# Kernel optimization log

Measured on AMD Instinct MI355X. Metric: run time of the kernel, lower is better.

## Reference

```python
import jax, jax.numpy as jnp
import numpy as np

WINDOW = 20  # window_size from init

def setup_inputs() -> dict:
    key = jax.random.key(0)
    ks = jax.random.split(key, 8)
    B, K, L, H = 8, 64, 1024, 256
    FFN = 3 * H * 4  # input_dim*ffn_ratio
    cand_span_reps = jax.random.normal(ks[0], (B, K, H), dtype=jnp.float32)
    token_reps = jax.random.normal(ks[1], (B, L, H), dtype=jnp.float32)
    W1 = jax.random.normal(ks[2], (3 * H, FFN), dtype=jnp.float32) * (1.0 / np.sqrt(3 * H))
    b1 = jnp.zeros((FFN,), dtype=jnp.float32)
    W2 = jax.random.normal(ks[3], (FFN, H), dtype=jnp.float32) * (1.0 / np.sqrt(FFN))
    b2 = jnp.zeros((H,), dtype=jnp.float32)
    cand_span_ids = jnp.sort(jax.random.randint(ks[4], (B, K, 2), 0, L), axis=-1)
    token_masks = jnp.ones((B, L), dtype=bool)
    return {"cand_span_reps": cand_span_reps, "token_reps": token_reps,
            "W1": W1, "b1": b1, "W2": W2, "b2": b2,
            "cand_span_ids": cand_span_ids, "token_masks": token_masks}

def _span_window_max(token_reps, span_ids, token_masks, window):
    # token_reps: [B,L,H]; span_ids: [B,K,2]; token_masks: [B,L]
    L = token_reps.shape[1]
    seq = jnp.arange(L)[None, None, :]                      # [1,1,L]
    start = span_ids[:, :, 0][:, :, None]                   # [B,K,1]
    end = span_ids[:, :, 1][:, :, None]                     # [B,K,1]
    mask = (((seq >= start - window) & (seq < start)) |
            ((seq > end) & (seq <= end + window)))
    mask = mask & token_masks[:, None, :]                   # [B,K,L]
    # masked max over L -> [B,K,H]
    filled = jnp.where(mask[..., None], token_reps[:, None, :, :], -jnp.inf)
    return jnp.max(filled, axis=2)

def reference(cand_span_reps, token_reps, W1, b1, W2, b2, cand_span_ids, token_masks):
    B, K, H = cand_span_reps.shape
    # Per-span pooled window context [B,K,H]. The pairwise context over the
    # UNION of head & tail windows equals the elementwise max of the two
    # per-span window maxes (max over A|B == max(max A, max B)).
    ctx = _span_window_max(token_reps, cand_span_ids, token_masks, WINDOW)
    context_reps = jnp.maximum(ctx[:, :, None, :], ctx[:, None, :, :])   # [B,K,K,H]
    head_reps = jnp.broadcast_to(cand_span_reps[:, :, None, :], (B, K, K, H))
    tail_reps = jnp.broadcast_to(cand_span_reps[:, None, :, :], (B, K, K, H))
    rel = jnp.concatenate([head_reps, tail_reps, context_reps], axis=-1)  # [B,K,K,3H]
    h = jax.nn.relu(jnp.einsum('bijd,df->bijf', rel, W1) + b1)
    out = jnp.einsum('bijf,fh->bijh', h, W2) + b2
    return out.reshape(B, K * K, H)
```

## Files before the change

kernel.cpp:

```cpp
#include <hip/hip_runtime.h>
#include <hip/hip_bf16.h>
#include <cstdint>
#include <cstddef>


typedef __attribute__((ext_vector_type(8))) short short8;
typedef __attribute__((ext_vector_type(4))) float f32x4;
typedef __attribute__((ext_vector_type(2))) unsigned int u32x2;

#define B_DIM 8
#define K_DIM 64
#define H_DIM 256
#define L_DIM 1024
#define FFN_DIM 3072
#define WINDOW 20

__device__ __forceinline__ unsigned short f2b(float f) {
  unsigned int u = __float_as_uint(f);
  unsigned int r = (u + 0x7FFFu + ((u >> 16) & 1u)) >> 16;
  return (unsigned short)r;
}
__device__ __forceinline__ float b2f(unsigned short h) {
  return __uint_as_float(((unsigned int)h) << 16);
}
__device__ __forceinline__ f32x4 zero4() {
  f32x4 z = {0.f, 0.f, 0.f, 0.f};
  return z;
}
__device__ __forceinline__ void gload_lds16(const void* g, void* l) {
  __builtin_amdgcn_global_load_lds(
      (const __attribute__((address_space(1))) void*)g,
      (__attribute__((address_space(3))) void*)l, 16, 0, 0);
}
__device__ __forceinline__ unsigned int cvt_pk_bf16(float lo, float hi) {
  unsigned int r;
  asm("v_cvt_pk_bf16_f32 %0, %1, %2" : "=v"(r) : "v"(lo), "v"(hi));
  return r;
}


__global__ void cvt_bf16_kernel(const float* __restrict__ in,
                                unsigned short* __restrict__ out, int n) {
  int i = blockIdx.x * blockDim.x + threadIdx.x;
  if (i < n) out[i] = f2b(in[i]);
}

__global__ void transpose_cvt_kernel(const float* __restrict__ in,
                                     unsigned short* __restrict__ out,
                                     int R, int C) {
  __shared__ float t[64][65];
  int c0 = blockIdx.x * 64, r0 = blockIdx.y * 64;
  int tr = threadIdx.x >> 6, tc = threadIdx.x & 63;
  for (int rr = tr; rr < 64; rr += 4)
    t[rr][tc] = in[(size_t)(r0 + rr) * C + (c0 + tc)];
  __syncthreads();
  for (int cc = tr; cc < 64; cc += 4)
    out[(size_t)(c0 + cc) * R + (r0 + tc)] = f2b(t[tc][cc]);
}

__global__ void ctx_kernel(const float* __restrict__ token,
                           const int* __restrict__ ids,
                           unsigned short* __restrict__ ctx) {
  int bk = blockIdx.x;
  int b = bk >> 6;
  int h = threadIdx.x;
  int s = ids[bk * 2 + 0];
  int e = ids[bk * 2 + 1];
  const float* tb = token + ((size_t)b * L_DIM) * H_DIM + h;
  float m = -INFINITY;
  int lo = s - WINDOW; if (lo < 0) lo = 0;
  for (int l2 = lo; l2 < s; ++l2) m = fmaxf(m, tb[(size_t)l2 * H_DIM]);
  int hi = e + WINDOW; if (hi > L_DIM - 1) hi = L_DIM - 1;
  for (int l2 = e + 1; l2 <= hi; ++l2) m = fmaxf(m, tb[(size_t)l2 * H_DIM]);
  ctx[(size_t)bk * H_DIM + h] = f2b(m);
}

__global__ __launch_bounds__(256) void at_gemm_kernel(
    const unsigned short* __restrict__ candb,
    const unsigned short* __restrict__ w1abt,
    const float* __restrict__ b1, float* __restrict__ AT) {
  int n0 = blockIdx.x * 64;
  int r0 = blockIdx.y * 64;
  __shared__ __align__(16) unsigned short A[64 * 256];
  int w = threadIdx.x >> 6, l = threadIdx.x & 63;
  int l15 = l & 15, l4 = l >> 4;
  {
    int row = w * 16 + l15;
    const short8* src = (const short8*)(candb + (size_t)(r0 + row) * H_DIM);
    #pragma unroll
    for (int t = 0; t < 8; ++t) {
      int u = l4 + 4 * t;
      short8 v = src[u];
      *(short8*)(A + row * 256 + ((u ^ (row & 7)) * 8)) = v;
    }
  }
  __syncthreads();
  f32x4 acc[4] = {zero4(), zero4(), zero4(), zero4()};
  int n = n0 + 16 * w + l15;
  const unsigned short* bp = w1abt + (size_t)n * H_DIM + l4 * 8;
  #pragma unroll
  for (int kk = 0; kk < 8; ++kk) {
    short8 bfrag = *(const short8*)(bp + kk * 32);
    #pragma unroll
    for (int rf = 0; rf < 4; ++rf) {
      int row = rf * 16 + l15;
      int u = kk * 4 + l4;
      short8 afrag = *(const short8*)(A + row * 256 + ((u ^ (row & 7)) * 8));
      acc[rf] = __builtin_amdgcn_mfma_f32_16x16x32_bf16(afrag, bfrag, acc[rf], 0, 0, 0);
    }
  }
  float bias = (n < FFN_DIM) ? b1[n] : 0.0f;
  #pragma unroll
  for (int rf = 0; rf < 4; ++rf) {
    #pragma unroll
    for (int qq = 0; qq < 4; ++qq) {
      int row = r0 + rf * 16 + l4 * 4 + qq;
      AT[(size_t)row * (2 * FFN_DIM) + n] = acc[rf][qq] + bias;
    }
  }
}

__global__ __launch_bounds__(512, 4) void fused_kernel(
    const unsigned short* __restrict__ ctx,
    const unsigned short* __restrict__ w1ct,
    const unsigned short* __restrict__ w2t,
    const float* __restrict__ AT,
    const float* __restrict__ b2,
    float* __restrict__ out) {
  int blk = blockIdx.x;
  blk = (blk & 7) * 64 + (blk >> 3);
  int b = blk >> 6, i = blk & 63;

  __shared__ __align__(16) char W1s[2 * 16384];
  __shared__ __align__(16) char W2s[2 * 16384];
  __shared__ __align__(16) char HcS[2 * 4096];

  int tid = threadIdx.x;
  int w = tid >> 6, l = tid & 63;
  int l15 = l & 15, l4 = l >> 4;
  int wl = l15 & 7;
  int s3 = (l15 >> 1) & 3;

  if (w < 4) {
    int wf = w & 1, wj2 = w >> 1;
    int jloc = 32 * wj2 + l15;

    short8 bfr[8][2];
    {
      const unsigned short* cb = ctx + ((size_t)b * K_DIM) * H_DIM;
      const unsigned short* ci = cb + (size_t)i * H_DIM;
      #pragma unroll
      for (int kk = 0; kk < 8; ++kk) {
        int hoff = kk * 32 + l4 * 8;
        short8 vi = *(const short8*)(ci + hoff);
        #pragma unroll
        for (int jb = 0; jb < 2; ++jb) {
          short8 vj = *(const short8*)(cb + (size_t)(jloc + jb * 16) * H_DIM + hoff);
          short8 vm;
          #pragma unroll
          for (int e = 0; e < 8; ++e) {
            float fa = b2f((unsigned short)vi[e]);
            float fb = b2f((unsigned short)vj[e]);
            vm[e] = (fa >= fb) ? vi[e] : vj[e];
          }
          bfr[kk][jb] = vm;
        }
      }
    }

    int baseA = (16 * wf + l15) * 512;
    int offAe = (l4 ^ wl) << 4;
    int offAo = ((4 + l4) ^ wl) << 4;
    int uW = 2 * wf + (l4 >> 1);
    int offHw = jloc * 64 + ((uW ^ s3) << 4) + ((l4 & 1) << 3);

    const float* avp  = AT + (size_t)(b * K_DIM + i) * (2 * FFN_DIM) + 16 * wf + 4 * l4;
    const float* tvp0 = AT + (size_t)(b * K_DIM + jloc) * (2 * FFN_DIM) + FFN_DIM + 16 * wf + 4 * l4;
    const float* tvp1 = tvp0 + (size_t)16 * (2 * FFN_DIM);

    __builtin_amdgcn_s_barrier();
    __builtin_amdgcn_sched_barrier(0);

    for (int c = 0; c <= 96; ++c) {
      if (c < 96) {
        f32x4 av  = *(const f32x4*)avp;
        f32x4 tv0 = *(const f32x4*)tvp0;
        f32x4 tv1 = *(const f32x4*)tvp1;
        avp += 32; tvp0 += 32; tvp1 += 32;
        __builtin_amdgcn_sched_barrier(0);

        const char* w1p = &W1s[(c & 1) * 16384 + baseA];
        f32x4 acc1[2] = {zero4(), zero4()};
        __builtin_amdgcn_s_setprio(1);
        #pragma unroll
        for (int m = 0; m < 4; ++m) {
          short8 afe = *(const short8*)(w1p + m * 128 + offAe);
          acc1[0] = __builtin_amdgcn_mfma_f32_16x16x32_bf16(afe, bfr[2 * m][0], acc1[0], 0, 0, 0);
          acc1[1] = __builtin_amdgcn_mfma_f32_16x16x32_bf16(afe, bfr[2 * m][1], acc1[1], 0, 0, 0);
          short8 afo = *(const short8*)(w1p + m * 128 + offAo);
          acc1[0] = __builtin_amdgcn_mfma_f32_16x16x32_bf16(afo, bfr[2 * m + 1][0], acc1[0], 0, 0, 0);
          acc1[1] = __builtin_amdgcn_mfma_f32_16x16x32_bf16(afo, bfr[2 * m + 1][1], acc1[1], 0, 0, 0);
        }
        __builtin_amdgcn_s_setprio(0);

        char* hw = &HcS[(c & 1) * 4096];
        {
          float v0 = fmaxf(acc1[0][0] + av[0] + tv0[0], 0.0f);
          float v1 = fmaxf(acc1[0][1] + av[1] + tv0[1], 0.0f);
          float v2 = fmaxf(acc1[0][2] + av[2] + tv0[2], 0.0f);
          float v3 = fmaxf(acc1[0][3] + av[3] + tv0[3], 0.0f);
          u32x2 pk;
          pk.x = cvt_pk_bf16(v0, v1);
          pk.y = cvt_pk_bf16(v2, v3);
          *(u32x2*)(hw + offHw) = pk;
        }
        {
          float v0 = fmaxf(acc1[1][0] + av[0] + tv1[0], 0.0f);
          float v1 = fmaxf(acc1[1][1] + av[1] + tv1[1], 0.0f);
          float v2 = fmaxf(acc1[1][2] + av[2] + tv1[2], 0.0f);
          float v3 = fmaxf(acc1[1][3] + av[3] + tv1[3], 0.0f);
          u32x2 pk;
          pk.x = cvt_pk_bf16(v0, v1);
          pk.y = cvt_pk_bf16(v2, v3);
          *(u32x2*)(hw + offHw + 1024) = pk;
        }
      }

      __builtin_amdgcn_sched_barrier(0);
      asm volatile("s_waitcnt vmcnt(0) lgkmcnt(0)" ::: "memory");
      __builtin_amdgcn_sched_barrier(0);
      __builtin_amdgcn_s_barrier();
      __builtin_amdgcn_sched_barrier(0);
    }
  } else {
    int ch = w - 4;
    int tid_c = (ch << 6) | l;

    int fr = tid_c >> 5, u32i = tid_c & 31;
    int offW1 = fr * 512 + (((u32i & 24) | ((u32i & 7) ^ (fr & 7))) << 4);
    int h2 = tid_c >> 2, u2 = tid_c & 3;
    int offW2 = h2 * 6144 + ((u2 ^ ((h2 >> 1) & 3)) << 4);

    const char* gW1 = (const char*)w1ct + offW1;
    const char* gW2 = (const char*)w2t + offW2;
    char* dW1base = &W1s[tid_c * 16];
    char* dW2base = &W2s[tid_c * 16];

    int baseW2 = ch * 4096 + l15 * 64 + ((l4 ^ s3) << 4);
    int baseHr = l15 * 64 + ((l4 ^ s3) << 4);

    f32x4 accO[4][4];
    #pragma unroll
    for (int cf = 0; cf < 4; ++cf)
      #pragma unroll
      for (int jt = 0; jt < 4; ++jt) accO[cf][jt] = zero4();

    {
      gload_lds16(gW1, dW1base);
      gload_lds16(gW1 + 4096, dW1base + 4096);
      gload_lds16(gW1 + 8192, dW1base + 8192);
      gload_lds16(gW1 + 12288, dW1base + 12288);
      gW1 += 16384;
    }
    __builtin_amdgcn_sched_barrier(0);
    asm volatile("s_waitcnt vmcnt(0)" ::: "memory");
    __builtin_amdgcn_sched_barrier(0);
    __builtin_amdgcn_s_barrier();
    __builtin_amdgcn_sched_barrier(0);

    for (int c = 0; c <= 96; ++c) {
      if (c < 95) {
        char* d = dW1base + ((c + 1) & 1) * 16384;
        gload_lds16(gW1, d);
        gload_lds16(gW1 + 4096, d + 4096);
        gload_lds16(gW1 + 8192, d + 8192);
        gload_lds16(gW1 + 12288, d + 12288);
        gW1 += 16384;
      }
      if (c < 96) {
        char* d = dW2base + (c & 1) * 16384;
        gload_lds16(gW2, d);
        gload_lds16(gW2 + 1 * 393216, d + 4096);
        gload_lds16(gW2 + 2 * 393216, d + 8192);
        gload_lds16(gW2 + 3 * 393216, d + 12288);
        gW2 += 64;
      }
      __builtin_amdgcn_sched_barrier(0);

      if (c > 0) {
        const char* w2p = &W2s[((c - 1) & 1) * 16384];
        const char* hcp = &HcS[((c - 1) & 1) * 4096];
        short8 wfr[4], hbv[4];
        #pragma unroll
        for (int cf = 0; cf < 4; ++cf)
          wfr[cf] = *(const short8*)(w2p + baseW2 + cf * 1024);
        #pragma unroll
        for (int jt = 0; jt < 4; ++jt)
          hbv[jt] = *(const short8*)(hcp + baseHr + jt * 1024);
        __builtin_amdgcn_s_setprio(1);
        #pragma unroll
        for (int cf = 0; cf < 4; ++cf)
          #pragma unroll
          for (int jt = 0; jt < 4; ++jt)
            accO[cf][jt] = __builtin_amdgcn_mfma_f32_16x16x32_bf16(wfr[cf], hbv[jt], accO[cf][jt], 0, 0, 0);
        __builtin_amdgcn_s_setprio(0);
      }

      __builtin_amdgcn_sched_barrier(0);
      asm volatile("s_waitcnt vmcnt(0) lgkmcnt(0)" ::: "memory");
      __builtin_amdgcn_sched_barrier(0);
      __builtin_amdgcn_s_barrier();
      __builtin_amdgcn_sched_barrier(0);
    }

    f32x4 bv[4];
    #pragma unroll
    for (int cf = 0; cf < 4; ++cf)
      bv[cf] = *(const f32x4*)(b2 + 64 * ch + cf * 16 + 4 * l4);
    #pragma unroll
    for (int jt = 0; jt < 4; ++jt) {
      int j = jt * 16 + l15;
      float* row = out + ((size_t)b * (K_DIM * K_DIM) + (size_t)i * K_DIM + j) * H_DIM;
      #pragma unroll
      for (int cf = 0; cf < 4; ++cf) {
        f32x4 v = accO[cf][jt] + bv[cf];
        *(f32x4*)(row + 64 * ch + cf * 16 + 4 * l4) = v;
      }
    }
  }
}


extern "C" void kernel_launch(void* const* d_in, const int* in_sizes, int n_in,
                              void* d_out, int out_size, void* d_ws, size_t ws_size,
                              hipStream_t stream) {
  const float* cand  = (const float*)d_in[0];
  const float* token = (const float*)d_in[1];
  const float* W1    = (const float*)d_in[2];
  const float* b1    = (const float*)d_in[3];
  const float* W2    = (const float*)d_in[4];
  const float* b2    = (const float*)d_in[5];
  const int*   ids   = (const int*)d_in[6];
  float* out = (float*)d_out;

  char* ws = (char*)d_ws;
  unsigned short* ctx   = (unsigned short*)(ws);
  unsigned short* candb = (unsigned short*)(ws + 262144);
  unsigned short* w1abt = (unsigned short*)(ws + 524288);
  unsigned short* w1ct  = (unsigned short*)(ws + 3670016);
  unsigned short* w2t   = (unsigned short*)(ws + 5242880);
  float*          AT    = (float*)(ws + 6815744);

  hipLaunchKernelGGL(cvt_bf16_kernel, dim3(512), dim3(256), 0, stream,
                     cand, candb, B_DIM * K_DIM * H_DIM);
  hipLaunchKernelGGL(transpose_cvt_kernel, dim3(48, 4), dim3(256), 0, stream,
                     W1, w1abt, 256, FFN_DIM);
  hipLaunchKernelGGL(transpose_cvt_kernel, dim3(48, 4), dim3(256), 0, stream,
                     W1 + (size_t)256 * FFN_DIM, w1abt + (size_t)FFN_DIM * 256, 256, FFN_DIM);
  hipLaunchKernelGGL(transpose_cvt_kernel, dim3(48, 4), dim3(256), 0, stream,
                     W1 + (size_t)512 * FFN_DIM, w1ct, 256, FFN_DIM);
  hipLaunchKernelGGL(transpose_cvt_kernel, dim3(4, 48), dim3(256), 0, stream,
                     W2, w2t, FFN_DIM, 256);
  hipLaunchKernelGGL(ctx_kernel, dim3(512), dim3(256), 0, stream, token, ids, ctx);
  hipLaunchKernelGGL(at_gemm_kernel, dim3(96, 8), dim3(256), 0, stream,
                     candb, w1abt, b1, AT);
  hipLaunchKernelGGL(fused_kernel, dim3(512), dim3(512), 0, stream,
                     ctx, w1ct, w2t, AT, b2, out);
}
```

Before: 181.2 us.

## Load W2 fragments directly into registers instead of staging through LDS

The consumer waves now read W2 MFMA fragments straight from global memory into double-buffered registers (even/odd), and the 32 KB W2 LDS buffer is removed. The loop is unrolled by two so each buffer is refilled one step ahead, and the wait becomes vmcnt(4) so the in-flight W2 loads can overlap the barrier. This removes an LDS write/read round trip and frees shared memory, which could raise occupancy. In exchange it issues uncoalesced 16-byte strided global loads (rows are FFN_DIM apart) that depend on L2 hits, and it assumes the vmcnt ordering is correct.

```diff
diff --git a/kernel.cpp b/kernel.cpp
--- a/kernel.cpp
+++ b/kernel.cpp
@@ -132,7 +132,6 @@
   int b = blk >> 6, i = blk & 63;
 
   __shared__ __align__(16) char W1s[2 * 16384];
-  __shared__ __align__(16) char W2s[2 * 16384];
   __shared__ __align__(16) char HcS[2 * 4096];
 
   int tid = threadIdx.x;
@@ -238,15 +237,11 @@
 
     int fr = tid_c >> 5, u32i = tid_c & 31;
     int offW1 = fr * 512 + (((u32i & 24) | ((u32i & 7) ^ (fr & 7))) << 4);
-    int h2 = tid_c >> 2, u2 = tid_c & 3;
-    int offW2 = h2 * 6144 + ((u2 ^ ((h2 >> 1) & 3)) << 4);
-
     const char* gW1 = (const char*)w1ct + offW1;
-    const char* gW2 = (const char*)w2t + offW2;
     char* dW1base = &W1s[tid_c * 16];
-    char* dW2base = &W2s[tid_c * 16];
-
-    int baseW2 = ch * 4096 + l15 * 64 + ((l4 ^ s3) << 4);
+
+    const unsigned short* w2r = w2t + (size_t)(64 * ch + l15) * FFN_DIM + l4 * 8;
+
     int baseHr = l15 * 64 + ((l4 ^ s3) << 4);
 
     f32x4 accO[4][4];
@@ -255,62 +250,73 @@
       #pragma unroll
       for (int jt = 0; jt < 4; ++jt) accO[cf][jt] = zero4();
 
-    {
-      gload_lds16(gW1, dW1base);
-      gload_lds16(gW1 + 4096, dW1base + 4096);
-      gload_lds16(gW1 + 8192, dW1base + 8192);
-      gload_lds16(gW1 + 12288, dW1base + 12288);
+    short8 wfE[4], wfO[4];
+
+    auto stageW1 = [&](char* d) {
+      gload_lds16(gW1, d);
+      gload_lds16(gW1 + 4096, d + 4096);
+      gload_lds16(gW1 + 8192, d + 8192);
+      gload_lds16(gW1 + 12288, d + 12288);
       gW1 += 16384;
-    }
-    __builtin_amdgcn_sched_barrier(0);
-    asm volatile("s_waitcnt vmcnt(0)" ::: "memory");
-    __builtin_amdgcn_sched_barrier(0);
-    __builtin_amdgcn_s_barrier();
-    __builtin_amdgcn_sched_barrier(0);
-
-    for (int c = 0; c <= 96; ++c) {
-      if (c < 95) {
-        char* d = dW1base + ((c + 1) & 1) * 16384;
-        gload_lds16(gW1, d);
-        gload_lds16(gW1 + 4096, d + 4096);
-        gload_lds16(gW1 + 8192, d + 8192);
-        gload_lds16(gW1 + 12288, d + 12288);
-        gW1 += 16384;
-      }
-      if (c < 96) {
-        char* d = dW2base + (c & 1) * 16384;
-        gload_lds16(gW2, d);
-        gload_lds16(gW2 + 1 * 393216, d + 4096);
-        gload_lds16(gW2 + 2 * 393216, d + 8192);
-        gload_lds16(gW2 + 3 * 393216, d + 12288);
-        gW2 += 64;
-      }
-      __builtin_amdgcn_sched_barrier(0);
-
-      if (c > 0) {
-        const char* w2p = &W2s[((c - 1) & 1) * 16384];
-        const char* hcp = &HcS[((c - 1) & 1) * 4096];
-        short8 wfr[4], hbv[4];
-        #pragma unroll
-        for (int cf = 0; cf < 4; ++cf)
-          wfr[cf] = *(const short8*)(w2p + baseW2 + cf * 1024);
+    };
+    auto loadW2 = [&](short8 (&buf)[4]) {
+      buf[0] = *(const short8*)(w2r);
+      buf[1] = *(const short8*)(w2r + (size_t)16 * FFN_DIM);
+      buf[2] = *(const short8*)(w2r + (size_t)32 * FFN_DIM);
+      buf[3] = *(const short8*)(w2r + (size_t)48 * FFN_DIM);
+      w2r += 32;
+    };
+    auto runG2 = [&](int cprev, short8 (&wfr)[4]) {
+      const char* hcp = &HcS[(cprev & 1) * 4096];
+      short8 hbv[4];
+      #pragma unroll
+      for (int jt = 0; jt < 4; ++jt)
+        hbv[jt] = *(const short8*)(hcp + baseHr + jt * 1024);
+      __builtin_amdgcn_s_setprio(1);
+      #pragma unroll
+      for (int cf = 0; cf < 4; ++cf)
         #pragma unroll
         for (int jt = 0; jt < 4; ++jt)
-          hbv[jt] = *(const short8*)(hcp + baseHr + jt * 1024);
-        __builtin_amdgcn_s_setprio(1);
-        #pragma unroll
-        for (int cf = 0; cf < 4; ++cf)
-          #pragma unroll
-          for (int jt = 0; jt < 4; ++jt)
-            accO[cf][jt] = __builtin_amdgcn_mfma_f32_16x16x32_bf16(wfr[cf], hbv[jt], accO[cf][jt], 0, 0, 0);
-        __builtin_amdgcn_s_setprio(0);
-      }
-
-      __builtin_amdgcn_sched_barrier(0);
-      asm volatile("s_waitcnt vmcnt(0) lgkmcnt(0)" ::: "memory");
+          accO[cf][jt] = __builtin_amdgcn_mfma_f32_16x16x32_bf16(wfr[cf], hbv[jt], accO[cf][jt], 0, 0, 0);
+      __builtin_amdgcn_s_setprio(0);
+    };
+    auto endbar = [&]() {
+      __builtin_amdgcn_sched_barrier(0);
+      asm volatile("s_waitcnt vmcnt(4) lgkmcnt(0)" ::: "memory");
       __builtin_amdgcn_sched_barrier(0);
       __builtin_amdgcn_s_barrier();
       __builtin_amdgcn_sched_barrier(0);
+    };
+
+    stageW1(dW1base);
+    loadW2(wfE);
+    __builtin_amdgcn_sched_barrier(0);
+    asm volatile("s_waitcnt vmcnt(0)" ::: "memory");
+    __builtin_amdgcn_sched_barrier(0);
+    __builtin_amdgcn_s_barrier();
+    __builtin_amdgcn_sched_barrier(0);
+
+    stageW1(dW1base + 16384);
+    __builtin_amdgcn_sched_barrier(0);
+    loadW2(wfO);
+    endbar();
+
+    for (int p = 0; p < 48; ++p) {
+      int c1 = 2 * p + 1;
+      if (c1 + 1 <= 95) stageW1(dW1base + (((c1 + 1) & 1) * 16384));
+      __builtin_amdgcn_sched_barrier(0);
+      runG2(c1 - 1, wfE);
+      __builtin_amdgcn_sched_barrier(0);
+      if (c1 + 1 <= 95) loadW2(wfE);
+      endbar();
+
+      int c2 = 2 * p + 2;
+      if (c2 + 1 <= 95) stageW1(dW1base + (((c2 + 1) & 1) * 16384));
+      __builtin_amdgcn_sched_barrier(0);
+      runG2(c2 - 1, wfO);
+      __builtin_amdgcn_sched_barrier(0);
+      if (c2 + 1 <= 95) loadW2(wfO);
+      endbar();
     }
 
     f32x4 bv[4];
```

Result: slower. 224.5 us (+23.9%).

## Halve GEMM1 producer waves and store head/tail FFN partials as bf16

Applied to the files above, without the earlier changes.

The fused kernel drops from four to two first-stage producer waves. Each producer now covers all 64 j-rows, issuing four MFMA accumulators per W1 fragment and holding twice the context fragments in registers. The block shrinks to 384 threads with launch bounds allowing three blocks per CU. The precomputed head/tail partial activations (AT) are written and read as bf16 instead of fp32, which halves that global traffic but adds rounding error before the ReLU.

```diff
diff --git a/kernel.cpp b/kernel.cpp
--- a/kernel.cpp
+++ b/kernel.cpp
@@ -7,6 +7,7 @@
 typedef __attribute__((ext_vector_type(8))) short short8;
 typedef __attribute__((ext_vector_type(4))) float f32x4;
 typedef __attribute__((ext_vector_type(2))) unsigned int u32x2;
+typedef __attribute__((ext_vector_type(4))) unsigned short u16x4;
 
 #define B_DIM 8
 #define K_DIM 64
@@ -78,7 +79,7 @@
 __global__ __launch_bounds__(256) void at_gemm_kernel(
     const unsigned short* __restrict__ candb,
     const unsigned short* __restrict__ w1abt,
-    const float* __restrict__ b1, float* __restrict__ AT) {
+    const float* __restrict__ b1, unsigned short* __restrict__ ATb) {
   int n0 = blockIdx.x * 64;
   int r0 = blockIdx.y * 64;
   __shared__ __align__(16) unsigned short A[64 * 256];
@@ -115,16 +116,16 @@
     #pragma unroll
     for (int qq = 0; qq < 4; ++qq) {
       int row = r0 + rf * 16 + l4 * 4 + qq;
-      AT[(size_t)row * (2 * FFN_DIM) + n] = acc[rf][qq] + bias;
+      ATb[(size_t)row * (2 * FFN_DIM) + n] = f2b(acc[rf][qq] + bias);
     }
   }
 }
 
-__global__ __launch_bounds__(512, 4) void fused_kernel(
+__global__ __launch_bounds__(384, 3) void fused_kernel(
     const unsigned short* __restrict__ ctx,
     const unsigned short* __restrict__ w1ct,
     const unsigned short* __restrict__ w2t,
-    const float* __restrict__ AT,
+    const unsigned short* __restrict__ ATb,
     const float* __restrict__ b2,
     float* __restrict__ out) {
   int blk = blockIdx.x;
@@ -141,11 +142,10 @@
   int wl = l15 & 7;
   int s3 = (l15 >> 1) & 3;
 
-  if (w < 4) {
-    int wf = w & 1, wj2 = w >> 1;
-    int jloc = 32 * wj2 + l15;
-
-    short8 bfr[8][2];
+  if (w < 2) {
+    int wf = w;
+
+    short8 bfr[8][4];
     {
       const unsigned short* cb = ctx + ((size_t)b * K_DIM) * H_DIM;
       const unsigned short* ci = cb + (size_t)i * H_DIM;
@@ -154,8 +154,8 @@
         int hoff = kk * 32 + l4 * 8;
         short8 vi = *(const short8*)(ci + hoff);
         #pragma unroll
-        for (int jb = 0; jb < 2; ++jb) {
-          short8 vj = *(const short8*)(cb + (size_t)(jloc + jb * 16) * H_DIM + hoff);
+        for (int jb = 0; jb < 4; ++jb) {
+          short8 vj = *(const short8*)(cb + (size_t)(jb * 16 + l15) * H_DIM + hoff);
           short8 vm;
           #pragma unroll
           for (int e = 0; e < 8; ++e) {
@@ -172,58 +172,75 @@
     int offAe = (l4 ^ wl) << 4;
     int offAo = ((4 + l4) ^ wl) << 4;
     int uW = 2 * wf + (l4 >> 1);
-    int offHw = jloc * 64 + ((uW ^ s3) << 4) + ((l4 & 1) << 3);
-
-    const float* avp  = AT + (size_t)(b * K_DIM + i) * (2 * FFN_DIM) + 16 * wf + 4 * l4;
-    const float* tvp0 = AT + (size_t)(b * K_DIM + jloc) * (2 * FFN_DIM) + FFN_DIM + 16 * wf + 4 * l4;
-    const float* tvp1 = tvp0 + (size_t)16 * (2 * FFN_DIM);
+    int offHw = l15 * 64 + ((uW ^ s3) << 4) + ((l4 & 1) << 3);
+
+    const unsigned short* avp = ATb + (size_t)(b * K_DIM + i) * (2 * FFN_DIM) + 16 * wf + 4 * l4;
+    const unsigned short* tvp = ATb + (size_t)(b * K_DIM + l15) * (2 * FFN_DIM) + FFN_DIM + 16 * wf + 4 * l4;
 
     __builtin_amdgcn_s_barrier();
     __builtin_amdgcn_sched_barrier(0);
 
     for (int c = 0; c <= 96; ++c) {
       if (c < 96) {
-        f32x4 av  = *(const f32x4*)avp;
-        f32x4 tv0 = *(const f32x4*)tvp0;
-        f32x4 tv1 = *(const f32x4*)tvp1;
-        avp += 32; tvp0 += 32; tvp1 += 32;
+        u16x4 avb = *(const u16x4*)avp;
+        u16x4 tvb0 = *(const u16x4*)(tvp);
+        u16x4 tvb1 = *(const u16x4*)(tvp + (size_t)16 * (2 * FFN_DIM));
+        u16x4 tvb2 = *(const u16x4*)(tvp + (size_t)32 * (2 * FFN_DIM));
+        u16x4 tvb3 = *(const u16x4*)(tvp + (size_t)48 * (2 * FFN_DIM));
+        avp += 32; tvp += 32;
         __builtin_amdgcn_sched_barrier(0);
 
         const char* w1p = &W1s[(c & 1) * 16384 + baseA];
-        f32x4 acc1[2] = {zero4(), zero4()};
+        f32x4 acc1[4] = {zero4(), zero4(), zero4(), zero4()};
         __builtin_amdgcn_s_setprio(1);
         #pragma unroll
         for (int m = 0; m < 4; ++m) {
           short8 afe = *(const short8*)(w1p + m * 128 + offAe);
-          acc1[0] = __builtin_amdgcn_mfma_f32_16x16x32_bf16(afe, bfr[2 * m][0], acc1[0], 0, 0, 0);
-          acc1[1] = __builtin_amdgcn_mfma_f32_16x16x32_bf16(afe, bfr[2 * m][1], acc1[1], 0, 0, 0);
+          #pragma unroll
+          for (int jb = 0; jb < 4; ++jb)
+            acc1[jb] = __builtin_amdgcn_mfma_f32_16x16x32_bf16(afe, bfr[2 * m][jb], acc1[jb], 0, 0, 0);
           short8 afo = *(const short8*)(w1p + m * 128 + offAo);
-          acc1[0] = __builtin_amdgcn_mfma_f32_16x16x32_bf16(afo, bfr[2 * m + 1][0], acc1[0], 0, 0, 0);
-          acc1[1] = __builtin_amdgcn_mfma_f32_16x16x32_bf16(afo, bfr[2 * m + 1][1], acc1[1], 0, 0, 0);
+          #pragma unroll
+          for (int jb = 0; jb < 4; ++jb)
+            acc1[jb] = __builtin_amdgcn_mfma_f32_16x16x32_bf16(afo, bfr[2 * m + 1][jb], acc1[jb], 0, 0, 0);
         }
         __builtin_amdgcn_s_setprio(0);
 
+        float a0 = b2f(avb[0]), a1 = b2f(avb[1]);
+        float a2 = b2f(avb[2]), a3 = b2f(avb[3]);
         char* hw = &HcS[(c & 1) * 4096];
         {
-          float v0 = fmaxf(acc1[0][0] + av[0] + tv0[0], 0.0f);
-          float v1 = fmaxf(acc1[0][1] + av[1] + tv0[1], 0.0f);
-          float v2 = fmaxf(acc1[0][2] + av[2] + tv0[2], 0.0f);
-          float v3 = fmaxf(acc1[0][3] + av[3] + tv0[3], 0.0f);
-          u32x2 pk;
-          pk.x = cvt_pk_bf16(v0, v1);
-          pk.y = cvt_pk_bf16(v2, v3);
+          float v0 = fmaxf(acc1[0][0] + a0 + b2f(tvb0[0]), 0.0f);
+          float v1 = fmaxf(acc1[0][1] + a1 + b2f(tvb0[1]), 0.0f);
+          float v2 = fmaxf(acc1[0][2] + a2 + b2f(tvb0[2]), 0.0f);
+          float v3 = fmaxf(acc1[0][3] + a3 + b2f(tvb0[3]), 0.0f);
+          u32x2 pk; pk.x = cvt_pk_bf16(v0, v1); pk.y = cvt_pk_bf16(v2, v3);
           *(u32x2*)(hw + offHw) = pk;
         }
         {
-          float v0 = fmaxf(acc1[1][0] + av[0] + tv1[0], 0.0f);
-          float v1 = fmaxf(acc1[1][1] + av[1] + tv1[1], 0.0f);
-          float v2 = fmaxf(acc1[1][2] + av[2] + tv1[2], 0.0f);
-          float v3 = fmaxf(acc1[1][3] + av[3] + tv1[3], 0.0f);
-          u32x2 pk;
-          pk.x = cvt_pk_bf16(v0, v1);
-          pk.y = cvt_pk_bf16(v2, v3);
+          float v0 = fmaxf(acc1[1][0] + a0 + b2f(tvb1[0]), 0.0f);
+          float v1 = fmaxf(acc1[1][1] + a1 + b2f(tvb1[1]), 0.0f);
+          float v2 = fmaxf(acc1[1][2] + a2 + b2f(tvb1[2]), 0.0f);
+          float v3 = fmaxf(acc1[1][3] + a3 + b2f(tvb1[3]), 0.0f);
+          u32x2 pk; pk.x = cvt_pk_bf16(v0, v1); pk.y = cvt_pk_bf16(v2, v3);
           *(u32x2*)(hw + offHw + 1024) = pk;
         }
+        {
+          float v0 = fmaxf(acc1[2][0] + a0 + b2f(tvb2[0]), 0.0f);
+          float v1 = fmaxf(acc1[2][1] + a1 + b2f(tvb2[1]), 0.0f);
+          float v2 = fmaxf(acc1[2][2] + a2 + b2f(tvb2[2]), 0.0f);
+          float v3 = fmaxf(acc1[2][3] + a3 + b2f(tvb2[3]), 0.0f);
+          u32x2 pk; pk.x = cvt_pk_bf16(v0, v1); pk.y = cvt_pk_bf16(v2, v3);
+          *(u32x2*)(hw + offHw + 2048) = pk;
+        }
+        {
+          float v0 = fmaxf(acc1[3][0] + a0 + b2f(tvb3[0]), 0.0f);
+          float v1 = fmaxf(acc1[3][1] + a1 + b2f(tvb3[1]), 0.0f);
+          float v2 = fmaxf(acc1[3][2] + a2 + b2f(tvb3[2]), 0.0f);
+          float v3 = fmaxf(acc1[3][3] + a3 + b2f(tvb3[3]), 0.0f);
+          u32x2 pk; pk.x = cvt_pk_bf16(v0, v1); pk.y = cvt_pk_bf16(v2, v3);
+          *(u32x2*)(hw + offHw + 3072) = pk;
+        }
       }
 
       __builtin_amdgcn_sched_barrier(0);
@@ -233,7 +250,7 @@
       __builtin_amdgcn_sched_barrier(0);
     }
   } else {
-    int ch = w - 4;
+    int ch = w - 2;
     int tid_c = (ch << 6) | l;
 
     int fr = tid_c >> 5, u32i = tid_c & 31;
@@ -349,7 +366,7 @@
   unsigned short* w1abt = (unsigned short*)(ws + 524288);
   unsigned short* w1ct  = (unsigned short*)(ws + 3670016);
   unsigned short* w2t   = (unsigned short*)(ws + 5242880);
-  float*          AT    = (float*)(ws + 6815744);
+  unsigned short* ATb   = (unsigned short*)(ws + 6815744);
 
   hipLaunchKernelGGL(cvt_bf16_kernel, dim3(512), dim3(256), 0, stream,
                      cand, candb, B_DIM * K_DIM * H_DIM);
@@ -363,7 +380,7 @@
                      W2, w2t, FFN_DIM, 256);
   hipLaunchKernelGGL(ctx_kernel, dim3(512), dim3(256), 0, stream, token, ids, ctx);
   hipLaunchKernelGGL(at_gemm_kernel, dim3(96, 8), dim3(256), 0, stream,
-                     candb, w1abt, b1, AT);
-  hipLaunchKernelGGL(fused_kernel, dim3(512), dim3(512), 0, stream,
-                     ctx, w1ct, w2t, AT, b2, out);
-}
+                     candb, w1abt, b1, ATb);
+  hipLaunchKernelGGL(fused_kernel, dim3(512), dim3(384), 0, stream,
+                     ctx, w1ct, w2t, ATb, b2, out);
+}
```

Measured after the change: 290.5 us. 1.6x slower.

## Load W1 context fragments directly from global memory instead of LDS staging

Applied to the files above, without the earlier changes.

The compute waves now read W1 context-weight fragments straight from global memory (through the cache) with per-lane vector loads, instead of having the consumer waves stage them into a double-buffered LDS tile via global-to-LDS copies. This drops 32KB of LDS per block and the W1 prefetch traffic from the second wave group, which could raise occupancy and shorten the barrier-bound loop. In exchange, global load latency now sits directly in front of the MFMA chain on the critical path, and every block re-fetches W1 from L2 rather than sharing one staged copy.

```diff
diff --git a/kernel.cpp b/kernel.cpp
--- a/kernel.cpp
+++ b/kernel.cpp
@@ -131,14 +131,12 @@
   blk = (blk & 7) * 64 + (blk >> 3);
   int b = blk >> 6, i = blk & 63;
 
-  __shared__ __align__(16) char W1s[2 * 16384];
   __shared__ __align__(16) char W2s[2 * 16384];
   __shared__ __align__(16) char HcS[2 * 4096];
 
   int tid = threadIdx.x;
   int w = tid >> 6, l = tid & 63;
   int l15 = l & 15, l4 = l >> 4;
-  int wl = l15 & 7;
   int s3 = (l15 >> 1) & 3;
 
   if (w < 4) {
@@ -168,9 +166,8 @@
       }
     }
 
-    int baseA = (16 * wf + l15) * 512;
-    int offAe = (l4 ^ wl) << 4;
-    int offAo = ((4 + l4) ^ wl) << 4;
+    const char* gW1a = (const char*)w1ct + (size_t)(16 * wf + l15) * 512 + l4 * 16;
+
     int uW = 2 * wf + (l4 >> 1);
     int offHw = jloc * 64 + ((uW ^ s3) << 4) + ((l4 & 1) << 3);
 
@@ -189,19 +186,19 @@
         avp += 32; tvp0 += 32; tvp1 += 32;
         __builtin_amdgcn_sched_barrier(0);
 
-        const char* w1p = &W1s[(c & 1) * 16384 + baseA];
         f32x4 acc1[2] = {zero4(), zero4()};
         __builtin_amdgcn_s_setprio(1);
         #pragma unroll
         for (int m = 0; m < 4; ++m) {
-          short8 afe = *(const short8*)(w1p + m * 128 + offAe);
+          short8 afe = *(const short8*)(gW1a + m * 128);
           acc1[0] = __builtin_amdgcn_mfma_f32_16x16x32_bf16(afe, bfr[2 * m][0], acc1[0], 0, 0, 0);
           acc1[1] = __builtin_amdgcn_mfma_f32_16x16x32_bf16(afe, bfr[2 * m][1], acc1[1], 0, 0, 0);
-          short8 afo = *(const short8*)(w1p + m * 128 + offAo);
+          short8 afo = *(const short8*)(gW1a + m * 128 + 64);
           acc1[0] = __builtin_amdgcn_mfma_f32_16x16x32_bf16(afo, bfr[2 * m + 1][0], acc1[0], 0, 0, 0);
           acc1[1] = __builtin_amdgcn_mfma_f32_16x16x32_bf16(afo, bfr[2 * m + 1][1], acc1[1], 0, 0, 0);
         }
         __builtin_amdgcn_s_setprio(0);
+        gW1a += 16384;
 
         char* hw = &HcS[(c & 1) * 4096];
         {
@@ -236,14 +233,9 @@
     int ch = w - 4;
     int tid_c = (ch << 6) | l;
 
-    int fr = tid_c >> 5, u32i = tid_c & 31;
-    int offW1 = fr * 512 + (((u32i & 24) | ((u32i & 7) ^ (fr & 7))) << 4);
     int h2 = tid_c >> 2, u2 = tid_c & 3;
     int offW2 = h2 * 6144 + ((u2 ^ ((h2 >> 1) & 3)) << 4);
-
-    const char* gW1 = (const char*)w1ct + offW1;
     const char* gW2 = (const char*)w2t + offW2;
-    char* dW1base = &W1s[tid_c * 16];
     char* dW2base = &W2s[tid_c * 16];
 
     int baseW2 = ch * 4096 + l15 * 64 + ((l4 ^ s3) << 4);
@@ -255,28 +247,10 @@
       #pragma unroll
       for (int jt = 0; jt < 4; ++jt) accO[cf][jt] = zero4();
 
-    {
-      gload_lds16(gW1, dW1base);
-      gload_lds16(gW1 + 4096, dW1base + 4096);
-      gload_lds16(gW1 + 8192, dW1base + 8192);
-      gload_lds16(gW1 + 12288, dW1base + 12288);
-      gW1 += 16384;
-    }
-    __builtin_amdgcn_sched_barrier(0);
-    asm volatile("s_waitcnt vmcnt(0)" ::: "memory");
-    __builtin_amdgcn_sched_barrier(0);
     __builtin_amdgcn_s_barrier();
     __builtin_amdgcn_sched_barrier(0);
 
     for (int c = 0; c <= 96; ++c) {
-      if (c < 95) {
-        char* d = dW1base + ((c + 1) & 1) * 16384;
-        gload_lds16(gW1, d);
-        gload_lds16(gW1 + 4096, d + 4096);
-        gload_lds16(gW1 + 8192, d + 8192);
-        gload_lds16(gW1 + 12288, d + 12288);
-        gW1 += 16384;
-      }
       if (c < 96) {
         char* d = dW2base + (c & 1) * 16384;
         gload_lds16(gW2, d);
```

Result: slower. 313.1 us (+72.8%).
